# Performance work log

Measured on AMD Instinct MI355X. Metric: run time of the kernel, lower is better.

Reference implementation:

```python
import jax, jax.numpy as jnp
import numpy as np

B, T, E = 64, 512, 300
H = 150            # sent_gru_h_dim; bi-GRU output = 2H = 300
A = 128            # sent_att_dim
G = 64             # aspect_att_dim
NC = 5             # categories
NCV = 30           # total context vectors: tasks1-4,6-9 have 3, task5 has 6
CV_CAT = np.array([0]*9 + [1]*3 + [2]*6 + [3]*6 + [4]*6)   # u-category per cv
TASK_START = [0, 3, 6, 9, 12, 18, 21, 24, 27]
TASK_COUNT = [3, 3, 3, 3, 6, 3, 3, 3, 3]
TASK_CAT = [0, 0, 0, 1, 2, 3, 3, 4, 4]


def setup_inputs() -> dict:
    key = jax.random.key(0)
    ks = jax.random.split(key, 18)
    s = 0.05
    p = lambda k, sh: jax.random.normal(k, sh, jnp.float32) * s
    docs = jax.random.normal(ks[0], (B, T, E), jnp.float32)
    lengths = jax.random.randint(ks[1], (B,), 64, T + 1, jnp.int32)
    lengths = lengths.at[0].set(T)  # ensure padded width == max length (pad_packed semantics)
    return {
        'docs': docs,
        'doc_lengths': lengths,
        'gru_w_ih_f': p(ks[2], (NC, 3 * H, E)),
        'gru_w_hh_f': p(ks[3], (NC, 3 * H, H)),
        'gru_b_ih_f': p(ks[4], (NC, 3 * H)),
        'gru_b_hh_f': p(ks[5], (NC, 3 * H)),
        'gru_w_ih_b': p(ks[6], (NC, 3 * H, E)),
        'gru_w_hh_b': p(ks[7], (NC, 3 * H, H)),
        'gru_b_ih_b': p(ks[8], (NC, 3 * H)),
        'gru_b_hh_b': p(ks[9], (NC, 3 * H)),
        'ln_gamma': jnp.ones((NC, 2 * H), jnp.float32),
        'ln_beta': jnp.zeros((NC, 2 * H), jnp.float32),
        'sent_att_w': p(ks[10], (NC, A, 2 * H)),
        'sent_att_b': p(ks[11], (NC, A)),
        'group_att_w': p(ks[12], (NC, G, 2 * H)),
        'group_att_b': p(ks[13], (NC, G)),
        'task_cv_w': p(ks[14], (NCV, A)),
        'group_cv_w': p(ks[15], (9, G)),
    }


def _gru_dir(x, w_ih, w_hh, b_ih, b_hh):
    # x: [B,T,E] -> h: [B,T,H], torch GRU gate order (r,z,n)
    xp = jnp.einsum('bte,ge->btg', x, w_ih) + b_ih  # [B,T,3H]
    def step(h, xp_t):
        gh = h @ w_hh.T + b_hh
        xr, xz, xn = jnp.split(xp_t, 3, axis=-1)
        hr, hz, hn = jnp.split(gh, 3, axis=-1)
        r = jax.nn.sigmoid(xr + hr)
        z = jax.nn.sigmoid(xz + hz)
        n = jnp.tanh(xn + r * hn)
        h = (1 - z) * n + z * h
        return h, h
    h0 = jnp.zeros((x.shape[0], w_hh.shape[1]), x.dtype)
    _, hs = jax.lax.scan(step, h0, jnp.swapaxes(xp, 0, 1))
    return jnp.swapaxes(hs, 0, 1)


def reference(docs, doc_lengths, gru_w_ih_f, gru_w_hh_f, gru_b_ih_f, gru_b_hh_f,
              gru_w_ih_b, gru_w_hh_b, gru_b_ih_b, gru_b_hh_b, ln_gamma, ln_beta,
              sent_att_w, sent_att_b, group_att_w, group_att_b, task_cv_w, group_cv_w):
    # sort by length descending (as in forward)
    perm = jnp.argsort(-doc_lengths)
    L = doc_lengths[perm]
    x = docs[perm]
    t_idx = jnp.arange(T)[None, :]
    mask = (t_idx < L[:, None]).astype(x.dtype)  # [B,T]
    # per-row reversal of the valid prefix (packed bi-GRU backward-direction semantics)
    rev_idx = jnp.where(t_idx < L[:, None], L[:, None] - 1 - t_idx, t_idx)  # [B,T]
    def rev(a):
        return jnp.take_along_axis(a, rev_idx[:, :, None], axis=1)

    def bigru(wif, whf, bif, bhf, wib, whb, bib, bhb):
        hf = _gru_dir(x, wif, whf, bif, bhf)
        hb = rev(_gru_dir(rev(x), wib, whb, bib, bhb))
        return jnp.concatenate([hf, hb], axis=-1)  # [B,T,2H]

    h_all = jax.vmap(bigru)(gru_w_ih_f, gru_w_hh_f, gru_b_ih_f, gru_b_hh_f,
                            gru_w_ih_b, gru_w_hh_b, gru_b_ih_b, gru_b_hh_b)  # [5,B,T,2H]

    # LayerNorm (eps=1e-5) + tanh(Linear) -> attention keys u per category
    mu = h_all.mean(-1, keepdims=True)
    var = h_all.var(-1, keepdims=True)
    hn = (h_all - mu) / jnp.sqrt(var + 1e-5) * ln_gamma[:, None, None, :] + ln_beta[:, None, None, :]
    u = jnp.tanh(jnp.einsum('cbtd,cad->cbta', hn, sent_att_w) + sent_att_b[:, None, None, :])  # [5,B,T,A]

    # NOTE: original forward reuses h_i from the LAST loop iteration (cat5); pad_packed zero-pads
    h_pad = h_all[4] * mask[:, :, None]  # [B,T,2H]

    # masked softmax per context vector (calc_att: exp(e - global_max), zero-pad, normalize over time)
    neg = jnp.float32(-1e30)
    att_list = []
    for c in range(NC):
        idx = np.nonzero(CV_CAT == c)[0]
        e = jnp.einsum('bta,ka->kbt', u[c], task_cv_w[idx])           # [k,B,T]
        gmax = jnp.max(jnp.where(mask[None] > 0, e, neg), axis=(1, 2), keepdims=True)
        a = jnp.exp(e - gmax) * mask[None]
        att_list.append(a / a.sum(axis=2, keepdims=True))
    att = jnp.concatenate(att_list, axis=0)                            # [30,B,T]

    docv = jnp.einsum('kbt,btd->kbd', att, h_pad)                      # [30,B,2H]

    # group attention over the per-task doc vectors (calc_prod_att3/6)
    outs = []
    for t in range(9):
        d = docv[TASK_START[t]:TASK_START[t] + TASK_COUNT[t]]          # [n,B,2H]
        c = TASK_CAT[t]
        g = jnp.einsum('nbd,gd->nbg', d, group_att_w[c]) + group_att_b[c]
        e = jnp.tanh(g @ group_cv_w[t])                                # [n,B]
        w = jnp.exp(e)
        w = w / w.sum(axis=0, keepdims=True)
        outs.append((d * w[:, :, None]).sum(axis=0))                   # [B,2H]
    return jnp.stack(outs)                                             # [9,B,2H]
```

## Files before the change

### kernel.cpp

```cpp
#include <hip/hip_runtime.h>
#include <hip/hip_bf16.h>
#include <math.h>

#define B   64
#define T   512
#define E   300
#define H   150
#define G3  450
#define DH  300
#define A   128
#define NC  5
#define NCV 30
#define KP  320
#define G3P 480
#define LDA 328
#define CHK 64

__constant__ int cK0[NC]  = {0,9,12,18,24};
__constant__ int cKC[NC]  = {9,3,6,6,6};
__constant__ int cTS[9]   = {0,3,6,9,12,18,21,24,27};
__constant__ int cTC[9]   = {3,3,3,3,6,3,3,3,3};
__constant__ int cTCAT[9] = {0,0,0,1,2,3,3,4,4};

typedef __attribute__((ext_vector_type(8))) short short8v;
typedef __attribute__((ext_vector_type(4))) short short4v;
typedef __attribute__((ext_vector_type(4))) float f32x4;

__device__ __forceinline__ short f2bf(float v) {
  unsigned u = __builtin_bit_cast(unsigned, v);
  u += 0x7FFFu + ((u >> 16) & 1u);
  return (short)(u >> 16);
}
__device__ __forceinline__ float bf2f(short s) {
  unsigned u = ((unsigned)(unsigned short)s) << 16;
  return __builtin_bit_cast(float, u);
}
__device__ __forceinline__ void bar_lgkm() {
  asm volatile("s_waitcnt lgkmcnt(0)" ::: "memory");
  __builtin_amdgcn_s_barrier();
  __builtin_amdgcn_sched_barrier(0);
}
__device__ __forceinline__ float fast_sig(float x) {
  return __builtin_amdgcn_rcpf(1.f + __expf(-x));
}
__device__ __forceinline__ float fast_tanh(float x) {
  x = fminf(fmaxf(x, -15.f), 15.f);
  float ex = __expf(2.f * x);
  return (ex - 1.f) * __builtin_amdgcn_rcpf(ex + 1.f);
}

__global__ void k_perm(const int* __restrict__ len, int* __restrict__ perm,
                       int* __restrict__ Lp) {
  __shared__ int sp[B];
  int b = threadIdx.x;
  int lb = len[b];
  int rank = 0;
  for (int j = 0; j < B; j++) {
    int lj = len[j];
    rank += (lj > lb) || (lj == lb && j < b);
  }
  sp[rank] = b;
  __syncthreads();
  perm[b] = sp[b];
  Lp[b] = len[sp[b]];
}

__global__ __launch_bounds__(256) void k_prepx(const float* __restrict__ docs,
    short* __restrict__ DXH, short* __restrict__ DXL) {
  const int total = B * T * (KP / 8);
  for (int i = blockIdx.x * 256 + threadIdx.x; i < total; i += gridDim.x * 256) {
    int bt = i / (KP / 8), q = i - bt * (KP / 8);
    const float* src = docs + (size_t)bt * E + q * 8;
    short8v h{}, l{};
#pragma unroll
    for (int j = 0; j < 8; j++) {
      int e = q * 8 + j;
      float v = (e < E) ? src[j] : 0.f;
      short hi = f2bf(v);
      h[j] = hi; l[j] = f2bf(v - bf2f(hi));
    }
    *(short8v*)(DXH + (size_t)bt * KP + q * 8) = h;
    *(short8v*)(DXL + (size_t)bt * KP + q * 8) = l;
  }
}

__global__ __launch_bounds__(64) void k_prepw(const float* __restrict__ saw,
    const float* __restrict__ sab, const float* __restrict__ gamma,
    const float* __restrict__ beta, short* __restrict__ WGH,
    short* __restrict__ WGL, float* __restrict__ SG, float* __restrict__ CB) {
  const int blk = blockIdx.x;
  const int c = blk >> 7;
  const int lane = threadIdx.x;
  const float* wrow = saw + (size_t)blk * DH;
  float sg = 0.f, cbv = 0.f;
  for (int e = lane; e < KP; e += 64) {
    float wg = 0.f;
    if (e < DH) {
      float w = wrow[e];
      wg = w * gamma[c * DH + e];
      sg += wg;
      cbv += beta[c * DH + e] * w;
    }
    short hi = f2bf(wg);
    WGH[(size_t)blk * KP + e] = hi;
    WGL[(size_t)blk * KP + e] = f2bf(wg - bf2f(hi));
  }
#pragma unroll
  for (int off = 32; off; off >>= 1) { sg += __shfl_xor(sg, off); cbv += __shfl_xor(cbv, off); }
  if (lane == 0) { SG[blk] = sg; CB[blk] = cbv + sab[blk]; }
}

#define GRU_STEP(TS, CUR, XC)                                                   \
  do {                                                                          \
    short8v ah_[5], al_[5];                                                     \
    _Pragma("unroll") for (int sl = 0; sl < 5; sl++) {                          \
      ah_[sl] = *(const short8v*)&hfH[CUR][l15][sl * 32 + kg * 8];              \
      al_[sl] = *(const short8v*)&hfL[CUR][l15][sl * 32 + kg * 8];              \
    }                                                                           \
    const int tpre = ((TS) + 2 < CHK) ? (TS) + 2 : CHK - 1;                     \
    float xN[3][4];                                                             \
    _Pragma("unroll") for (int sec = 0; sec < 3; sec++)                         \
      _Pragma("unroll") for (int v = 0; v < 4; v++)                             \
        xN[sec][v] = XPg[xbase[v] + (size_t)tpre * G3P + sec * 160];            \
    f32x4 acc[3];                                                               \
    _Pragma("unroll") for (int sec = 0; sec < 3; sec++)                         \
      acc[sec] = f32x4{bias3[sec], bias3[sec], bias3[sec], bias3[sec]};         \
    _Pragma("unroll") for (int sl = 0; sl < 5; sl++) {                          \
      _Pragma("unroll") for (int sec = 0; sec < 3; sec++) {                     \
        acc[sec] = __builtin_amdgcn_mfma_f32_16x16x32_bf16(ah_[sl], Wf[sec][sl], acc[sec], 0, 0, 0); \
        acc[sec] = __builtin_amdgcn_mfma_f32_16x16x32_bf16(al_[sl], Wf[sec][sl], acc[sec], 0, 0, 0); \
      }                                                                         \
    }                                                                           \
    const int t = gtbase + (TS);                                                \
    _Pragma("unroll") for (int v = 0; v < 4; v++) {                             \
      float r = fast_sig(XC[0][v] + acc[0][v]);                                 \
      float z = fast_sig(XC[1][v] + acc[1][v]);                                 \
      float n = fast_tanh(fmaf(r, acc[2][v], XC[2][v]));                        \
      float hnew = fmaf(z, hq[v] - n, n);                                       \
      if (!uLive) hnew = 0.f;                                                   \
      hq[v] = hnew;                                                             \
      short hi = f2bf(hnew); float rem = hnew - bf2f(hi);                       \
      hfH[(CUR) ^ 1][kg * 4 + v][u] = hi;                                       \
      hfL[(CUR) ^ 1][kg * 4 + v][u] = f2bf(rem);                                \
      if (uLive) {                                                              \
        int tout = dir ? ((t < Lq[v]) ? (Lq[v] - 1 - t) : t) : t;               \
        HALL[ho[v] + (size_t)tout * DH] = __float2bfloat16(hnew);               \
      }                                                                         \
    }                                                                           \
    _Pragma("unroll") for (int sec = 0; sec < 3; sec++)                         \
      _Pragma("unroll") for (int v = 0; v < 4; v++) XC[sec][v] = xN[sec][v];    \
    bar_lgkm();                                                                 \
  } while (0)

template<int MODE>
__global__ __launch_bounds__(640, 1) void k_xg(int gtbase, int xtbase,
    const float* __restrict__ XPg, float* __restrict__ XPx,
    const short* __restrict__ DXH, const short* __restrict__ DXL,
    const float* __restrict__ wihf, const float* __restrict__ wihb,
    const float* __restrict__ bihf, const float* __restrict__ bihb,
    const float* __restrict__ whf, const float* __restrict__ whb,
    const float* __restrict__ bhf, const float* __restrict__ bhb,
    const int* __restrict__ perm, const int* __restrict__ Lp,
    __hip_bfloat16* __restrict__ HALL, float* __restrict__ HST) {
  extern __shared__ __align__(16) char smem[];
  const int tid = threadIdx.x, lane = tid & 63, wid = tid >> 6;
  const int l15 = lane & 15, kg = lane >> 4;
  bool isGru; int xpBlk;
  if (MODE == 0) { isGru = (int)blockIdx.x < 40; xpBlk = blockIdx.x - 40; }
  else if (MODE == 1) { isGru = false; xpBlk = blockIdx.x; }
  else { isGru = true; xpBlk = 0; }

  if (!isGru) {
    const int xcd = xpBlk & 7, i0 = xpBlk >> 3;
    const int y = 2 * xcd + (i0 >= 30 ? 1 : 0);
    const int sn = (i0 >= 30) ? i0 - 30 : i0;
    const int s = sn / 3, nt = sn - (sn / 3) * 3;
    const int c = s >> 1, dir = s & 1;
    const float* W  = (dir ? wihb : wihf) + (size_t)c * G3 * E;
    const float* Bi = (dir ? bihb : bihf) + (size_t)c * G3;
    const int u = wid * 16 + l15;
    const int gwp = nt * 160 + u;
    const bool gv = (u < H);
    const int g = nt * H + u;
    const float biasv = gv ? Bi[g] : 0.f;
    short8v Whi[10], Wlo[10];
#pragma unroll
    for (int sl = 0; sl < 10; sl++) {
      short8v hi{}, lo{};
      if (gv) {
#pragma unroll
        for (int j = 0; j < 8; j++) {
          int k = sl * 32 + kg * 8 + j;
          if (k < E) {
            float w = W[(size_t)g * E + k];
            short h = f2bf(w);
            hi[j] = h; lo[j] = f2bf(w - bf2f(h));
          }
        }
      }
      Whi[sl] = hi; Wlo[sl] = lo;
    }
    short* Ah = (short*)smem;
    short* Al = (short*)(smem + 32 * LDA * 2);
    for (int it = 0; it < 8; it++) {
      const int idx = y * 8 + it;
      const int b = idx >> 1, mtile = idx & 1;
      const int L = Lp[b];
      const int pb = perm[b];
      const int t0g = xtbase + mtile * 32;
      for (int f = tid; f < 32 * (KP / 8); f += 640) {
        int r = f / (KP / 8), q = f - r * (KP / 8);
        int tg = t0g + r;
        int src = (dir && tg < L) ? (L - 1 - tg) : tg;
        size_t go = ((size_t)pb * T + src) * KP + q * 8;
        *(short8v*)&Ah[r * LDA + q * 8] = *(const short8v*)(DXH + go);
        *(short8v*)&Al[r * LDA + q * 8] = *(const short8v*)(DXL + go);
      }
      __syncthreads();
      f32x4 acc0[2], acc1[2];
#pragma unroll
      for (int m2 = 0; m2 < 2; m2++) {
        acc0[m2] = f32x4{biasv, biasv, biasv, biasv};
        acc1[m2] = f32x4{0.f, 0.f, 0.f, 0.f};
      }
#pragma unroll
      for (int sl = 0; sl < 10; sl += 2) {
#pragma unroll
        for (int m2 = 0; m2 < 2; m2++) {
          const int ro0 = (m2 * 16 + l15) * LDA + sl * 32 + kg * 8;
          short8v ah0 = *(const short8v*)&Ah[ro0];
          short8v al0 = *(const short8v*)&Al[ro0];
          acc0[m2] = __builtin_amdgcn_mfma_f32_16x16x32_bf16(ah0, Whi[sl], acc0[m2], 0, 0, 0);
          acc0[m2] = __builtin_amdgcn_mfma_f32_16x16x32_bf16(ah0, Wlo[sl], acc0[m2], 0, 0, 0);
          acc0[m2] = __builtin_amdgcn_mfma_f32_16x16x32_bf16(al0, Whi[sl], acc0[m2], 0, 0, 0);
          const int ro1 = ro0 + 32;
          short8v ah1 = *(const short8v*)&Ah[ro1];
          short8v al1 = *(const short8v*)&Al[ro1];
          acc1[m2] = __builtin_amdgcn_mfma_f32_16x16x32_bf16(ah1, Whi[sl + 1], acc1[m2], 0, 0, 0);
          acc1[m2] = __builtin_amdgcn_mfma_f32_16x16x32_bf16(ah1, Wlo[sl + 1], acc1[m2], 0, 0, 0);
          acc1[m2] = __builtin_amdgcn_mfma_f32_16x16x32_bf16(al1, Whi[sl + 1], acc1[m2], 0, 0, 0);
        }
      }
      const size_t base = (size_t)(s * B + b) * CHK * G3P;
#pragma unroll
      for (int m2 = 0; m2 < 2; m2++) {
        f32x4 acc = acc0[m2] + acc1[m2];
        const int lt = mtile * 32 + m2 * 16 + kg * 4;
        float* xp = XPx + base + (size_t)lt * G3P + gwp;
#pragma unroll
        for (int v = 0; v < 4; v++) xp[(size_t)v * G3P] = acc[v];
      }
      __syncthreads();
    }
    return;
  }

  const int blk = blockIdx.x;
  const int s = blk >> 2, bt = blk & 3;
  const int b0 = bt << 4;
  const int c = s >> 1, dir = s & 1;
  const float* Whh = (dir ? whb : whf) + (size_t)c * G3 * H;
  const float* Bhh = (dir ? bhb : bhf) + (size_t)c * G3;
  short (*hfH)[16][168] = (short(*)[16][168])smem;
  short (*hfL)[16][168] = (short(*)[16][168])(smem + 10752);

  const int u = wid * 16 + l15;
  const bool uLive = (u < H);

  short8v Wf[3][5];
  float bias3[3];
#pragma unroll
  for (int sec = 0; sec < 3; sec++) {
    bias3[sec] = uLive ? Bhh[sec * H + u] : 0.f;
#pragma unroll
    for (int sl = 0; sl < 5; sl++) {
      short8v w = {};
      if (uLive) {
#pragma unroll
        for (int j = 0; j < 8; j++) {
          int k = sl * 32 + kg * 8 + j;
          if (k < H) w[j] = f2bf(Whh[(size_t)(sec * H + u) * H + k]);
        }
      }
      Wf[sec][sl] = w;
    }
  }

  float hq[4];
  int Lq[4];
  size_t xbase[4], ho[4];
#pragma unroll
  for (int v = 0; v < 4; v++) {
    int bg = b0 + kg * 4 + v;
    Lq[v] = Lp[bg];
    xbase[v] = ((size_t)(s * B + bg) * CHK) * G3P + u;
    ho[v] = ((size_t)(c * B + bg) * T) * DH + (size_t)dir * H + u;
    hq[v] = 0.f;
    if (gtbase > 0 && uLive) hq[v] = HST[(size_t)(s * B + bg) * 152 + u];
  }

  for (int f = tid; f < 2 * 16 * 168; f += 640) {
    ((short*)hfH)[f] = 0; ((short*)hfL)[f] = 0;
  }
  __syncthreads();
#pragma unroll
  for (int v = 0; v < 4; v++) {
    short hi = f2bf(hq[v]); float rem = hq[v] - bf2f(hi);
    hfH[0][kg * 4 + v][u] = hi;
    hfL[0][kg * 4 + v][u] = f2bf(rem);
  }
  float xA[3][4], xB[3][4];
#pragma unroll
  for (int sec = 0; sec < 3; sec++)
#pragma unroll
    for (int v = 0; v < 4; v++) {
      xA[sec][v] = XPg[xbase[v] + sec * 160];
      xB[sec][v] = XPg[xbase[v] + (size_t)G3P + sec * 160];
    }
  __syncthreads();

  for (int ts = 0; ts < CHK; ts += 2) {
    GRU_STEP(ts, 0, xA);
    GRU_STEP(ts + 1, 1, xB);
  }
  if (uLive) {
#pragma unroll
    for (int v = 0; v < 4; v++)
      HST[(size_t)(s * B + b0 + kg * 4 + v) * 152 + u] = hq[v];
  }
}

__global__ __launch_bounds__(512) void k_fuse(const __hip_bfloat16* __restrict__ HALL,
    const short* __restrict__ WGH, const short* __restrict__ WGL,
    const float* __restrict__ SG, const float* __restrict__ CB,
    const float* __restrict__ cvw, float* __restrict__ Ebuf) {
  const int c = blockIdx.y;
  const int b = blockIdx.x >> 2, quar = blockIdx.x & 3;
  const int tid = threadIdx.x, lane = tid & 63, wid = tid >> 6;
  const int l15 = lane & 15, kg = lane >> 4;
  __shared__ short hs[32 * LDA];
  __shared__ float mu_s[32], rs_s[32];
  __shared__ float U_s[32][132];

  const int n = wid * 16 + l15;
  const float sga = SG[c * A + n], cba = CB[c * A + n];
  short8v Wh[10], Wl[10];
#pragma unroll
  for (int sl = 0; sl < 10; sl++) {
    size_t go = ((size_t)(c * A + n)) * KP + sl * 32 + kg * 8;
    Wh[sl] = *(const short8v*)(WGH + go);
    Wl[sl] = *(const short8v*)(WGL + go);
  }
  const int kc = cKC[c], k0c = cK0[c];
  for (int tt = 0; tt < 4; tt++) {
    const int t0 = (quar * 4 + tt) * 32;
    const short* hbase = (const short*)HALL + ((size_t)(c * B + b) * T + t0) * DH;
    for (int f = tid; f < 32 * 80; f += 512) {
      int r = f / 80, g4 = f - r * 80;
      short4v v{};
      if (g4 < 75) v = *(const short4v*)(hbase + (size_t)r * DH + g4 * 4);
      *(short4v*)&hs[r * LDA + g4 * 4] = v;
    }
    __syncthreads();
    {
      int r = tid >> 4, l = tid & 15;
      float sm = 0.f, sq = 0.f;
      for (int e = l; e < DH; e += 16) {
        float v = bf2f(hs[r * LDA + e]); sm += v; sq += v * v;
      }
      sm += __shfl_xor(sm, 1); sm += __shfl_xor(sm, 2); sm += __shfl_xor(sm, 4); sm += __shfl_xor(sm, 8);
      sq += __shfl_xor(sq, 1); sq += __shfl_xor(sq, 2); sq += __shfl_xor(sq, 4); sq += __shfl_xor(sq, 8);
      if (l == 0) {
        float mu = sm * (1.f / 300.f);
        float var = fmaxf(sq * (1.f / 300.f) - mu * mu, 0.f);
        mu_s[r] = mu; rs_s[r] = rsqrtf(var + 1e-5f);
      }
    }
    __syncthreads();
    f32x4 acch[2] = {}, accl[2] = {};
#pragma unroll
    for (int sl = 0; sl < 10; sl++) {
#pragma unroll
      for (int m2 = 0; m2 < 2; m2++) {
        short8v ah = *(const short8v*)&hs[(m2 * 16 + l15) * LDA + sl * 32 + kg * 8];
        acch[m2] = __builtin_amdgcn_mfma_f32_16x16x32_bf16(ah, Wh[sl], acch[m2], 0, 0, 0);
        accl[m2] = __builtin_amdgcn_mfma_f32_16x16x32_bf16(ah, Wl[sl], accl[m2], 0, 0, 0);
      }
    }
#pragma unroll
    for (int m2 = 0; m2 < 2; m2++) {
      f32x4 acc = acch[m2] + accl[m2];
#pragma unroll
      for (int v = 0; v < 4; v++) {
        int row = m2 * 16 + kg * 4 + v;
        float val = rs_s[row] * acc[v] - mu_s[row] * rs_s[row] * sga + cba;
        U_s[row][n] = fast_tanh(val);
      }
    }
    __syncthreads();
    for (int idx = tid; idx < 32 * kc; idx += 512) {
      int r = idx / kc, kk = idx - r * kc;
      const float* cv = cvw + (size_t)(k0c + kk) * A;
      float e = 0.f;
#pragma unroll 4
      for (int a = 0; a < A; a++) e = fmaf(U_s[r][a], cv[a], e);
      Ebuf[((size_t)(k0c + kk) * B + b) * T + t0 + r] = e;
    }
    __syncthreads();
  }
}

__global__ __launch_bounds__(256) void k_soft(float* __restrict__ Ebuf,
    const int* __restrict__ Lp) {
  const int k = blockIdx.x >> 6, b = blockIdx.x & 63;
  const int L = Lp[b];
  float* er = Ebuf + ((size_t)k * B + b) * T;
  const int tid = threadIdx.x;
  float v0 = (tid < L) ? er[tid] : -1e30f;
  float v1 = (tid + 256 < L) ? er[tid + 256] : -1e30f;
  float mx = fmaxf(v0, v1);
  __shared__ float red[4];
  __shared__ float red2[4];
#pragma unroll
  for (int off = 32; off; off >>= 1) mx = fmaxf(mx, __shfl_xor(mx, off));
  if ((tid & 63) == 0) red[tid >> 6] = mx;
  __syncthreads();
  mx = fmaxf(fmaxf(red[0], red[1]), fmaxf(red[2], red[3]));
  float e0 = (tid < L) ? __expf(v0 - mx) : 0.f;
  float e1 = (tid + 256 < L) ? __expf(v1 - mx) : 0.f;
  float sm = e0 + e1;
#pragma unroll
  for (int off = 32; off; off >>= 1) sm += __shfl_xor(sm, off);
  if ((tid & 63) == 0) red2[tid >> 6] = sm;
  __syncthreads();
  sm = red2[0] + red2[1] + red2[2] + red2[3];
  const float inv = 1.f / sm;
  er[tid] = e0 * inv;
  er[tid + 256] = e1 * inv;
}

__global__ __launch_bounds__(256) void k_docv(const __hip_bfloat16* __restrict__ HALL,
    const float* __restrict__ ATT, float* __restrict__ DOCVP) {
  const int dt = blockIdx.x, b = blockIdx.y, tp = blockIdx.z;
  const int d0 = dt << 6, t0 = tp << 6;
  const int tid = threadIdx.x, tx = tid & 63, ky = tid >> 6;
  const __hip_bfloat16* hb_ = HALL + ((size_t)(4 * B + b) * T + t0) * DH;
  __shared__ float h_s[64][65];
  __shared__ float att_s[30][66];
  float acc[8] = {};
  const int d = d0 + tx;
  for (int f = tid; f < 64 * 64; f += 256) {
    int ttt = f >> 6, dl = f & 63;
    h_s[ttt][dl] = (d0 + dl < DH)
        ? __bfloat162float(hb_[(size_t)ttt * DH + d0 + dl]) : 0.f;
  }
  for (int f = tid; f < 30 * 64; f += 256) {
    int kk = f >> 6, ttt = f & 63;
    att_s[kk][ttt] = ATT[((size_t)kk * B + b) * T + t0 + ttt];
  }
  __syncthreads();
  for (int ttt = 0; ttt < 64; ttt++) {
    float hv = h_s[ttt][tx];
#pragma unroll
    for (int i = 0; i < 8; i++) {
      int kk = ky + (i << 2);
      if (kk < 30) acc[i] = fmaf(att_s[kk][ttt], hv, acc[i]);
    }
  }
  if (d < DH) {
#pragma unroll
    for (int i = 0; i < 8; i++) {
      int kk = ky + (i << 2);
      if (kk < 30)
        DOCVP[((size_t)(tp * NCV + kk) * B + b) * DH + d] = acc[i];
    }
  }
}

__global__ __launch_bounds__(256) void k_dred(const float* __restrict__ DOCVP,
    float* __restrict__ DOCV) {
  const int n4 = NCV * B * DH / 4;
  int i = blockIdx.x * 256 + threadIdx.x;
  if (i < n4) {
    f32x4 s = {};
#pragma unroll
    for (int p = 0; p < 8; p++) s += ((const f32x4*)DOCVP)[(size_t)p * n4 + i];
    ((f32x4*)DOCV)[i] = s;
  }
}

__global__ __launch_bounds__(64) void k_group(const float* __restrict__ DOCV,
    const float* __restrict__ gaw, const float* __restrict__ gab,
    const float* __restrict__ gcv, float* __restrict__ out) {
  const int tt = blockIdx.x / B, b = blockIdx.x % B;
  const int lane = threadIdx.x;
  const int c = cTCAT[tt], cnt = cTC[tt], ks = cTS[tt];
  const float* wrow = gaw + ((size_t)c * 64 + lane) * DH;
  const float gbias = gab[c * 64 + lane];
  const float cvl = gcv[tt * 64 + lane];
  float accd[5] = {0, 0, 0, 0, 0};
  float wsum = 0.f;
  for (int n = 0; n < cnt; n++) {
    const float* drow = DOCV + ((size_t)(ks + n) * B + b) * DH;
    float g = 0.f;
    for (int dd = 0; dd < DH; dd++) g = fmaf(drow[dd], wrow[dd], g);
    g += gbias;
    float p = g * cvl;
#pragma unroll
    for (int off = 32; off; off >>= 1) p += __shfl_xor(p, off);
    float w = __expf(tanhf(p));
    wsum += w;
#pragma unroll
    for (int i = 0; i < 5; i++) {
      int dd = lane + (i << 6);
      if (dd < DH) accd[i] = fmaf(w, drow[dd], accd[i]);
    }
  }
  const float inv = 1.f / wsum;
  float* orow = out + ((size_t)tt * B + b) * DH;
#pragma unroll
  for (int i = 0; i < 5; i++) {
    int dd = lane + (i << 6);
    if (dd < DH) orow[dd] = accd[i] * inv;
  }
}

extern "C" void kernel_launch(void* const* d_in, const int* in_sizes, int n_in,
                              void* d_out, int out_size, void* d_ws, size_t ws_size,
                              hipStream_t stream) {
  const float* docs = (const float*)d_in[0];
  const int* lens = (const int*)d_in[1];
  const float* wihf = (const float*)d_in[2];
  const float* whhf = (const float*)d_in[3];
  const float* bihf = (const float*)d_in[4];
  const float* bhhf = (const float*)d_in[5];
  const float* wihb = (const float*)d_in[6];
  const float* whhb = (const float*)d_in[7];
  const float* bihb = (const float*)d_in[8];
  const float* bhhb = (const float*)d_in[9];
  const float* gam = (const float*)d_in[10];
  const float* bet = (const float*)d_in[11];
  const float* saw = (const float*)d_in[12];
  const float* sab = (const float*)d_in[13];
  const float* gaw = (const float*)d_in[14];
  const float* gab = (const float*)d_in[15];
  const float* cvw = (const float*)d_in[16];
  const float* gcv = (const float*)d_in[17];
  float* out = (float*)d_out;

  char* ws = (char*)d_ws;
  size_t off = 0;
  auto alloc = [&](size_t bytes) { size_t o = off; off = (off + bytes + 255) & ~(size_t)255; return o; };
  int* PERM = (int*)(ws + alloc(64 * 4));
  int* LP   = (int*)(ws + alloc(64 * 4));
  __hip_bfloat16* HALL = (__hip_bfloat16*)(ws + alloc((size_t)NC * B * T * DH * 2));
  float* EB    = (float*)(ws + alloc((size_t)NCV * B * T * 4));
  float* DOCV  = (float*)(ws + alloc((size_t)NCV * B * DH * 4));
  float* DOCVP = (float*)(ws + alloc((size_t)8 * NCV * B * DH * 4));
  float* HST   = (float*)(ws + alloc((size_t)640 * 152 * 4));
  short* WGH   = (short*)(ws + alloc((size_t)NC * A * KP * 2));
  short* WGL   = (short*)(ws + alloc((size_t)NC * A * KP * 2));
  float* SG    = (float*)(ws + alloc((size_t)NC * A * 4));
  float* CB    = (float*)(ws + alloc((size_t)NC * A * 4));
  short* DXH   = (short*)(ws + alloc((size_t)B * T * KP * 2));
  short* DXL   = (short*)(ws + alloc((size_t)B * T * KP * 2));
  const size_t xpBytes = (size_t)10 * B * CHK * G3P * 4;
  const bool dbuf = (off + 2 * xpBytes + 512) <= ws_size;
  float* XP0 = (float*)(ws + alloc(xpBytes));
  float* XP1 = dbuf ? (float*)(ws + alloc(xpBytes)) : XP0;

  const int DYN = 32 * LDA * 2 * 2;
  const int NXP = 480;

  hipLaunchKernelGGL(k_perm, dim3(1), dim3(64), 0, stream, lens, PERM, LP);
  hipLaunchKernelGGL(k_prepx, dim3(2048), dim3(256), 0, stream, docs, DXH, DXL);
  hipLaunchKernelGGL(k_prepw, dim3(NC * A), dim3(64), 0, stream,
                     saw, sab, gam, bet, WGH, WGL, SG, CB);
  if (dbuf) {
    k_xg<1><<<dim3(NXP), dim3(640), DYN, stream>>>(0, 0,
        XP0, XP0, DXH, DXL, wihf, wihb, bihf, bihb,
        whhf, whhb, bhhf, bhhb, PERM, LP, HALL, HST);
    for (int j = 0; j < 7; j++) {
      float* g = (j & 1) ? XP1 : XP0;
      float* x = (j & 1) ? XP0 : XP1;
      k_xg<0><<<dim3(40 + NXP), dim3(640), DYN, stream>>>(j * CHK, (j + 1) * CHK,
          g, x, DXH, DXL, wihf, wihb, bihf, bihb,
          whhf, whhb, bhhf, bhhb, PERM, LP, HALL, HST);
    }
    k_xg<2><<<dim3(40), dim3(640), DYN, stream>>>(7 * CHK, 0,
        XP1, XP1, DXH, DXL, wihf, wihb, bihf, bihb,
        whhf, whhb, bhhf, bhhb, PERM, LP, HALL, HST);
  } else {
    for (int j = 0; j < 8; j++) {
      k_xg<1><<<dim3(NXP), dim3(640), DYN, stream>>>(0, j * CHK,
          XP0, XP0, DXH, DXL, wihf, wihb, bihf, bihb,
          whhf, whhb, bhhf, bhhb, PERM, LP, HALL, HST);
      k_xg<2><<<dim3(40), dim3(640), DYN, stream>>>(j * CHK, 0,
          XP0, XP0, DXH, DXL, wihf, wihb, bihf, bihb,
          whhf, whhb, bhhf, bhhb, PERM, LP, HALL, HST);
    }
  }
  hipLaunchKernelGGL(k_fuse, dim3(256, 5), dim3(512), 0, stream,
                     HALL, WGH, WGL, SG, CB, cvw, EB);
  hipLaunchKernelGGL(k_soft, dim3(1920), dim3(256), 0, stream, EB, LP);
  hipLaunchKernelGGL(k_docv, dim3(5, 64, 8), dim3(256), 0, stream, HALL, EB, DOCVP);
  hipLaunchKernelGGL(k_dred, dim3((NCV * B * DH / 4 + 255) / 256), dim3(256), 0, stream,
                     DOCVP, DOCV);
  hipLaunchKernelGGL(k_group, dim3(576), dim3(64), 0, stream, DOCV, gaw, gab, gcv, out);
}
```

Measured before the change: 1.750 ms.

## Merge prep kernels and prefetch next tiles into registers in xgen and fuse

```diff
diff --git a/kernel.cpp b/kernel.cpp
--- a/kernel.cpp
+++ b/kernel.cpp
@@ -49,26 +49,55 @@
   return (ex - 1.f) * __builtin_amdgcn_rcpf(ex + 1.f);
 }
 
-__global__ void k_perm(const int* __restrict__ len, int* __restrict__ perm,
-                       int* __restrict__ Lp) {
+__global__ __launch_bounds__(256) void k_prep(const float* __restrict__ docs,
+    const int* __restrict__ len, short* __restrict__ DXH, short* __restrict__ DXL,
+    const float* __restrict__ saw, const float* __restrict__ sab,
+    const float* __restrict__ gamma, const float* __restrict__ beta,
+    short* __restrict__ WGH, short* __restrict__ WGL,
+    float* __restrict__ SG, float* __restrict__ CB,
+    int* __restrict__ perm, int* __restrict__ Lp) {
+  const int tid = threadIdx.x;
   __shared__ int sp[B];
-  int b = threadIdx.x;
-  int lb = len[b];
-  int rank = 0;
-  for (int j = 0; j < B; j++) {
-    int lj = len[j];
-    rank += (lj > lb) || (lj == lb && j < b);
-  }
-  sp[rank] = b;
+  if (blockIdx.x == 0 && tid < B) {
+    int lb = len[tid];
+    int rank = 0;
+    for (int j = 0; j < B; j++) {
+      int lj = len[j];
+      rank += (lj > lb) || (lj == lb && j < tid);
+    }
+    sp[rank] = tid;
+  }
   __syncthreads();
-  perm[b] = sp[b];
-  Lp[b] = len[sp[b]];
-}
-
-__global__ __launch_bounds__(256) void k_prepx(const float* __restrict__ docs,
-    short* __restrict__ DXH, short* __restrict__ DXL) {
+  if (blockIdx.x == 0 && tid < B) {
+    perm[tid] = sp[tid];
+    Lp[tid] = len[sp[tid]];
+  }
+  if (blockIdx.x >= 1888) {
+    const int w = (blockIdx.x - 1888) * 4 + (tid >> 6);
+    const int lane = tid & 63;
+    if (w < NC * A) {
+      const int c = w >> 7;
+      const float* wrow = saw + (size_t)w * DH;
+      float sg = 0.f, cbv = 0.f;
+      for (int e = lane; e < KP; e += 64) {
+        float wg = 0.f;
+        if (e < DH) {
+          float wv = wrow[e];
+          wg = wv * gamma[c * DH + e];
+          sg += wg;
+          cbv += beta[c * DH + e] * wv;
+        }
+        short hi = f2bf(wg);
+        WGH[(size_t)w * KP + e] = hi;
+        WGL[(size_t)w * KP + e] = f2bf(wg - bf2f(hi));
+      }
+#pragma unroll
+      for (int off = 32; off; off >>= 1) { sg += __shfl_xor(sg, off); cbv += __shfl_xor(cbv, off); }
+      if (lane == 0) { SG[w] = sg; CB[w] = cbv + sab[w]; }
+    }
+  }
   const int total = B * T * (KP / 8);
-  for (int i = blockIdx.x * 256 + threadIdx.x; i < total; i += gridDim.x * 256) {
+  for (int i = blockIdx.x * 256 + tid; i < total; i += 2048 * 256) {
     int bt = i / (KP / 8), q = i - bt * (KP / 8);
     const float* src = docs + (size_t)bt * E + q * 8;
     short8v h{}, l{};
@@ -82,32 +111,6 @@
     *(short8v*)(DXH + (size_t)bt * KP + q * 8) = h;
     *(short8v*)(DXL + (size_t)bt * KP + q * 8) = l;
   }
-}
-
-__global__ __launch_bounds__(64) void k_prepw(const float* __restrict__ saw,
-    const float* __restrict__ sab, const float* __restrict__ gamma,
-    const float* __restrict__ beta, short* __restrict__ WGH,
-    short* __restrict__ WGL, float* __restrict__ SG, float* __restrict__ CB) {
-  const int blk = blockIdx.x;
-  const int c = blk >> 7;
-  const int lane = threadIdx.x;
-  const float* wrow = saw + (size_t)blk * DH;
-  float sg = 0.f, cbv = 0.f;
-  for (int e = lane; e < KP; e += 64) {
-    float wg = 0.f;
-    if (e < DH) {
-      float w = wrow[e];
-      wg = w * gamma[c * DH + e];
-      sg += wg;
-      cbv += beta[c * DH + e] * w;
-    }
-    short hi = f2bf(wg);
-    WGH[(size_t)blk * KP + e] = hi;
-    WGL[(size_t)blk * KP + e] = f2bf(wg - bf2f(hi));
-  }
-#pragma unroll
-  for (int off = 32; off; off >>= 1) { sg += __shfl_xor(sg, off); cbv += __shfl_xor(cbv, off); }
-  if (lane == 0) { SG[blk] = sg; CB[blk] = cbv + sab[blk]; }
 }
 
 #define GRU_STEP(TS, CUR, XC)                                                   \
@@ -202,21 +205,52 @@
     }
     short* Ah = (short*)smem;
     short* Al = (short*)(smem + 32 * LDA * 2);
-    for (int it = 0; it < 8; it++) {
-      const int idx = y * 8 + it;
-      const int b = idx >> 1, mtile = idx & 1;
-      const int L = Lp[b];
-      const int pb = perm[b];
-      const int t0g = xtbase + mtile * 32;
-      for (int f = tid; f < 32 * (KP / 8); f += 640) {
-        int r = f / (KP / 8), q = f - r * (KP / 8);
+    short8v rAh[2], rAl[2];
+    {
+      const int idx = y * 8;
+      const int bb = idx >> 1;
+      const int L = Lp[bb];
+      const int pb = perm[bb];
+      const int t0g = xtbase;
+#pragma unroll
+      for (int k2 = 0; k2 < 2; k2++) {
+        int f = tid + k2 * 640;
+        int r = f / 40, q = f - r * 40;
         int tg = t0g + r;
         int src = (dir && tg < L) ? (L - 1 - tg) : tg;
         size_t go = ((size_t)pb * T + src) * KP + q * 8;
-        *(short8v*)&Ah[r * LDA + q * 8] = *(const short8v*)(DXH + go);
-        *(short8v*)&Al[r * LDA + q * 8] = *(const short8v*)(DXL + go);
+        rAh[k2] = *(const short8v*)(DXH + go);
+        rAl[k2] = *(const short8v*)(DXL + go);
+      }
+    }
+    for (int it = 0; it < 8; it++) {
+      const int idx = y * 8 + it;
+      const int bb = idx >> 1, mtile = idx & 1;
+#pragma unroll
+      for (int k2 = 0; k2 < 2; k2++) {
+        int f = tid + k2 * 640;
+        int r = f / 40, q = f - r * 40;
+        *(short8v*)&Ah[r * LDA + q * 8] = rAh[k2];
+        *(short8v*)&Al[r * LDA + q * 8] = rAl[k2];
       }
       __syncthreads();
+      if (it + 1 < 8) {
+        const int idx2 = idx + 1;
+        const int b2 = idx2 >> 1, mt2 = idx2 & 1;
+        const int L2 = Lp[b2];
+        const int pb2 = perm[b2];
+        const int t0g2 = xtbase + mt2 * 32;
+#pragma unroll
+        for (int k2 = 0; k2 < 2; k2++) {
+          int f = tid + k2 * 640;
+          int r = f / 40, q = f - r * 40;
+          int tg = t0g2 + r;
+          int src = (dir && tg < L2) ? (L2 - 1 - tg) : tg;
+          size_t go = ((size_t)pb2 * T + src) * KP + q * 8;
+          rAh[k2] = *(const short8v*)(DXH + go);
+          rAl[k2] = *(const short8v*)(DXL + go);
+        }
+      }
       f32x4 acc0[2], acc1[2];
 #pragma unroll
       for (int m2 = 0; m2 < 2; m2++) {
@@ -241,7 +275,7 @@
           acc1[m2] = __builtin_amdgcn_mfma_f32_16x16x32_bf16(al1, Whi[sl + 1], acc1[m2], 0, 0, 0);
         }
       }
-      const size_t base = (size_t)(s * B + b) * CHK * G3P;
+      const size_t base = (size_t)(s * B + bb) * CHK * G3P;
 #pragma unroll
       for (int m2 = 0; m2 < 2; m2++) {
         f32x4 acc = acc0[m2] + acc1[m2];
@@ -335,7 +369,7 @@
     const float* __restrict__ SG, const float* __restrict__ CB,
     const float* __restrict__ cvw, float* __restrict__ Ebuf) {
   const int c = blockIdx.y;
-  const int b = blockIdx.x >> 2, quar = blockIdx.x & 3;
+  const int b = blockIdx.x >> 3, oct = blockIdx.x & 7;
   const int tid = threadIdx.x, lane = tid & 63, wid = tid >> 6;
   const int l15 = lane & 15, kg = lane >> 4;
   __shared__ short hs[32 * LDA];
@@ -352,21 +386,33 @@
     Wl[sl] = *(const short8v*)(WGL + go);
   }
   const int kc = cKC[c], k0c = cK0[c];
-  for (int tt = 0; tt < 4; tt++) {
-    const int t0 = (quar * 4 + tt) * 32;
-    const short* hbase = (const short*)HALL + ((size_t)(c * B + b) * T + t0) * DH;
-    for (int f = tid; f < 32 * 80; f += 512) {
-      int r = f / 80, g4 = f - r * 80;
-      short4v v{};
-      if (g4 < 75) v = *(const short4v*)(hbase + (size_t)r * DH + g4 * 4);
-      *(short4v*)&hs[r * LDA + g4 * 4] = v;
-    }
-    __syncthreads();
+  const short* hb0 = (const short*)HALL + ((size_t)(c * B + b) * T + oct * 64) * DH;
+  for (int f = tid; f < 32 * 80; f += 512) {
+    int r = f / 80, g4 = f - r * 80;
+    short4v v{};
+    if (g4 < 75) v = *(const short4v*)(hb0 + (size_t)r * DH + g4 * 4);
+    *(short4v*)&hs[r * LDA + g4 * 4] = v;
+  }
+  __syncthreads();
+  short4v rg[5];
+  for (int tt = 0; tt < 2; tt++) {
+    const int t0 = oct * 64 + tt * 32;
+    if (tt == 0) {
+      const short* hb1 = hb0 + (size_t)32 * DH;
+#pragma unroll
+      for (int j = 0; j < 5; j++) {
+        int f = tid + j * 512;
+        int r = f / 80, g4 = f - r * 80;
+        rg[j] = (g4 < 75) ? *(const short4v*)(hb1 + (size_t)r * DH + g4 * 4) : short4v{};
+      }
+    }
     {
       int r = tid >> 4, l = tid & 15;
       float sm = 0.f, sq = 0.f;
-      for (int e = l; e < DH; e += 16) {
-        float v = bf2f(hs[r * LDA + e]); sm += v; sq += v * v;
+      for (int sl8 = l; sl8 < 38; sl8 += 16) {
+        short8v v = *(const short8v*)&hs[r * LDA + sl8 * 8];
+#pragma unroll
+        for (int j = 0; j < 8; j++) { float fv = bf2f(v[j]); sm += fv; sq += fv * fv; }
       }
       sm += __shfl_xor(sm, 1); sm += __shfl_xor(sm, 2); sm += __shfl_xor(sm, 4); sm += __shfl_xor(sm, 8);
       sq += __shfl_xor(sq, 1); sq += __shfl_xor(sq, 2); sq += __shfl_xor(sq, 4); sq += __shfl_xor(sq, 8);
@@ -376,7 +422,6 @@
         mu_s[r] = mu; rs_s[r] = rsqrtf(var + 1e-5f);
       }
     }
-    __syncthreads();
     f32x4 acch[2] = {}, accl[2] = {};
 #pragma unroll
     for (int sl = 0; sl < 10; sl++) {
@@ -385,6 +430,15 @@
         short8v ah = *(const short8v*)&hs[(m2 * 16 + l15) * LDA + sl * 32 + kg * 8];
         acch[m2] = __builtin_amdgcn_mfma_f32_16x16x32_bf16(ah, Wh[sl], acch[m2], 0, 0, 0);
         accl[m2] = __builtin_amdgcn_mfma_f32_16x16x32_bf16(ah, Wl[sl], accl[m2], 0, 0, 0);
+      }
+    }
+    __syncthreads();
+    if (tt == 0) {
+#pragma unroll
+      for (int j = 0; j < 5; j++) {
+        int f = tid + j * 512;
+        int r = f / 80, g4 = f - r * 80;
+        *(short4v*)&hs[r * LDA + g4 * 4] = rg[j];
       }
     }
 #pragma unroll
@@ -572,10 +626,9 @@
   const int DYN = 32 * LDA * 2 * 2;
   const int NXP = 480;
 
-  hipLaunchKernelGGL(k_perm, dim3(1), dim3(64), 0, stream, lens, PERM, LP);
-  hipLaunchKernelGGL(k_prepx, dim3(2048), dim3(256), 0, stream, docs, DXH, DXL);
-  hipLaunchKernelGGL(k_prepw, dim3(NC * A), dim3(64), 0, stream,
-                     saw, sab, gam, bet, WGH, WGL, SG, CB);
+  hipLaunchKernelGGL(k_prep, dim3(2048), dim3(256), 0, stream,
+                     docs, lens, DXH, DXL, saw, sab, gam, bet,
+                     WGH, WGL, SG, CB, PERM, LP);
   if (dbuf) {
     k_xg<1><<<dim3(NXP), dim3(640), DYN, stream>>>(0, 0,
         XP0, XP0, DXH, DXL, wihf, wihb, bihf, bihb,
@@ -600,7 +653,7 @@
           whhf, whhb, bhhf, bhhb, PERM, LP, HALL, HST);
     }
   }
-  hipLaunchKernelGGL(k_fuse, dim3(256, 5), dim3(512), 0, stream,
+  hipLaunchKernelGGL(k_fuse, dim3(512, 5), dim3(512), 0, stream,
                      HALL, WGH, WGL, SG, CB, cvw, EB);
   hipLaunchKernelGGL(k_soft, dim3(1920), dim3(256), 0, stream, EB, LP);
   hipLaunchKernelGGL(k_docv, dim3(5, 64, 8), dim3(256), 0, stream, HALL, EB, DOCVP);
```

New measurement: 1.756 ms. About the same (+0.4%).
